# Kernel tuning notes

Hardware: AMD Instinct MI355X
Metric: run time of the kernel (lower is better)

## Reference

```python
import jax, jax.numpy as jnp
import numpy as np
from jax import lax

B, S, W = 64, 64, 12          # batch, sentences, words-per-sentence (max_seq)
V, SYM, HID = 32000, 128, 256  # vocab, symbol_size, hidden_size
E, R = 64, 32                  # entity_size, role_size
EPS = 1e-5


def _mlp(x, W1, b1, W2, b2):
    # equation 'b...e,er->b...r' is a matmul on the last axis; tanh hidden, linear out
    return jnp.tanh(x @ W1 + b1) @ W2 + b2


def _ln(x, g, b):
    mu = jnp.mean(x, axis=-1, keepdims=True)
    var = jnp.mean(jnp.square(x - mu), axis=-1, keepdims=True)
    return (x - mu) * lax.rsqrt(var + EPS) * g + b


def setup_inputs() -> dict:
    key = jax.random.key(0)
    ks = jax.random.split(key, 24)
    s_in = 1.0 / np.sqrt(SYM)
    s_h = 1.0 / np.sqrt(HID)
    inp = {
        "story": jax.random.randint(ks[0], (B, S, W), 0, V),
        "query": jax.random.randint(ks[1], (B, W), 0, V),
        "word_embed": jax.random.uniform(ks[2], (V, SYM), jnp.float32, -0.1, 0.1),
        "pos_embed": jnp.ones((W, SYM), jnp.float32) / W,
        # UpdateModule MLPs: 2 entity heads (out=E), 3 role heads (out=R), stacked
        "ue_W1": jax.random.normal(ks[3], (2, SYM, HID)) * s_in,
        "ue_b1": jnp.zeros((2, HID), jnp.float32),
        "ue_W2": jax.random.normal(ks[4], (2, HID, E)) * s_h,
        "ue_b2": jnp.zeros((2, E), jnp.float32),
        "ur_W1": jax.random.normal(ks[5], (3, SYM, HID)) * s_in,
        "ur_b1": jnp.zeros((3, HID), jnp.float32),
        "ur_W2": jax.random.normal(ks[6], (3, HID, R)) * s_h,
        "ur_b2": jnp.zeros((3, R), jnp.float32),
        # InferenceModule MLPs
        "ie_W1": jax.random.normal(ks[7], (2, SYM, HID)) * s_in,
        "ie_b1": jnp.zeros((2, HID), jnp.float32),
        "ie_W2": jax.random.normal(ks[8], (2, HID, E)) * s_h,
        "ie_b2": jnp.zeros((2, E), jnp.float32),
        "ir_W1": jax.random.normal(ks[9], (3, SYM, HID)) * s_in,
        "ir_b1": jnp.zeros((3, HID), jnp.float32),
        "ir_W2": jax.random.normal(ks[10], (3, HID, R)) * s_h,
        "ir_b2": jnp.zeros((3, R), jnp.float32),
        "ln_g": jnp.ones((3, E), jnp.float32),
        "ln_b": jnp.zeros((3, E), jnp.float32),
        "Z": jax.random.normal(ks[11], (E, V)) * (1.0 / np.sqrt(E)),
    }
    return inp


def reference(story, query, word_embed, pos_embed,
              ue_W1, ue_b1, ue_W2, ue_b2, ur_W1, ur_b1, ur_W2, ur_b2,
              ie_W1, ie_b1, ie_W2, ie_b2, ir_W1, ir_b1, ir_W2, ir_b2,
              ln_g, ln_b, Z):
    # ---- InputModule ----
    sent = jnp.einsum('bswe,we->bse', word_embed[story], pos_embed)   # [B,S,SYM]
    qsum = jnp.einsum('bwe,we->be', word_embed[query], pos_embed)     # [B,SYM]

    # ---- UpdateModule: precompute per-step entity/role vectors ----
    e1 = _mlp(sent, ue_W1[0], ue_b1[0], ue_W2[0], ue_b2[0])  # [B,S,E]
    e2 = _mlp(sent, ue_W1[1], ue_b1[1], ue_W2[1], ue_b2[1])
    r1 = _mlp(sent, ur_W1[0], ur_b1[0], ur_W2[0], ur_b2[0])  # [B,S,R]
    r2 = _mlp(sent, ur_W1[1], ur_b1[1], ur_W2[1], ur_b2[1])
    r3 = _mlp(sent, ur_W1[2], ur_b1[2], ur_W2[2], ur_b2[2])
    paW = jnp.einsum('bsr,bsf->bsrf', r1, e2)
    paB = jnp.einsum('bsr,bsf->bsrf', r3, e1)

    xs = tuple(jnp.moveaxis(t, 1, 0) for t in (e1, r1, paW, e2, r2, paB, r3))

    def step(TPR, x):
        e1i, r1i, paWi, e2i, r2i, paBi, r3i = x
        t1 = jnp.einsum('be,berf->brf', e1i, TPR)
        w_hat = jnp.einsum('br,brf->bf', r1i, t1)
        m_hat = jnp.einsum('br,brf->bf', r2i, t1)
        b_hat = jnp.einsum('be,br,berf->bf', e2i, r3i, TPR)
        write_op = paWi - r1i[:, :, None] * w_hat[:, None, :]
        move_op = r2i[:, :, None] * (w_hat - m_hat)[:, None, :]
        back_op = paBi - r3i[:, :, None] * b_hat[:, None, :]
        delta = (jnp.einsum('be,brf->berf', e1i, write_op + move_op)
                 + jnp.einsum('be,brf->berf', e2i, back_op))
        return TPR + delta, None

    TPR0 = jnp.zeros((sent.shape[0], E, R, E), sent.dtype)
    TPR, _ = lax.scan(step, TPR0, xs)

    # ---- InferenceModule ----
    qe1 = _mlp(qsum, ie_W1[0], ie_b1[0], ie_W2[0], ie_b2[0])
    qr1 = _mlp(qsum, ir_W1[0], ir_b1[0], ir_W2[0], ir_b2[0])
    qr2 = _mlp(qsum, ir_W1[1], ir_b1[1], ir_W2[1], ir_b2[1])
    qr3 = _mlp(qsum, ir_W1[2], ir_b1[2], ir_W2[2], ir_b2[2])
    i1 = _ln(jnp.einsum('be,br,berf->bf', qe1, qr1, TPR), ln_g[0], ln_b[0])
    i2 = _ln(jnp.einsum('be,br,berf->bf', i1, qr2, TPR), ln_g[1], ln_b[1])
    i3 = _ln(jnp.einsum('be,br,berf->bf', i2, qr3, TPR), ln_g[2], ln_b[2])
    return (i1 + i2 + i3) @ Z
```

## Files before the change

### kernel.cpp

```cpp
#include <hip/hip_runtime.h>
#include <math.h>

#define B_   64
#define S_   64
#define W_   12
#define V_   32000
#define SYM_ 128
#define HID_ 256
#define E_   64
#define R_   32

__global__ __launch_bounds__(128) void k_embed(
    const int* __restrict__ story, const int* __restrict__ query,
    const float* __restrict__ we, const float* __restrict__ pe,
    float* __restrict__ X) {
  int row = blockIdx.x;
  int e = threadIdx.x;
  const int* idx = (row < 4096) ? story + row * W_ : query + (row - 4096) * W_;
  float acc = 0.f;
#pragma unroll
  for (int w = 0; w < W_; ++w)
    acc = fmaf(we[(long)idx[w] * SYM_ + e], pe[w * SYM_ + e], acc);
  X[row * SYM_ + e] = acc;
}

__global__ __launch_bounds__(256) void k_mlp(
    const float* __restrict__ X,
    const float* __restrict__ ueW1, const float* __restrict__ ueb1,
    const float* __restrict__ ueW2, const float* __restrict__ ueb2,
    const float* __restrict__ urW1, const float* __restrict__ urb1,
    const float* __restrict__ urW2, const float* __restrict__ urb2,
    const float* __restrict__ ieW1, const float* __restrict__ ieb1,
    const float* __restrict__ ieW2, const float* __restrict__ ieb2,
    const float* __restrict__ irW1, const float* __restrict__ irb1,
    const float* __restrict__ irW2, const float* __restrict__ irb2,
    float* __restrict__ oE0, float* __restrict__ oE1,
    float* __restrict__ oR0, float* __restrict__ oR1, float* __restrict__ oR2) {
  __shared__ float SM[9472];
  float* W1L = SM + 1280;

  int h = blockIdx.x % 5;
  int tile = blockIdx.x / 5;
  int rowbase = tile * 32;
  bool isQ = (rowbase >= 4096);
  bool isE = (h < 2);
  const float* W1 = isE ? (isQ ? ieW1 : ueW1) + h * (SYM_ * HID_)
                        : (isQ ? irW1 : urW1) + (h - 2) * (SYM_ * HID_);
  const float* b1 = isE ? (isQ ? ieb1 : ueb1) + h * HID_
                        : (isQ ? irb1 : urb1) + (h - 2) * HID_;
  const float* W2 = isE ? (isQ ? ieW2 : ueW2) + h * (HID_ * E_)
                        : (isQ ? irW2 : urW2) + (h - 2) * (HID_ * R_);
  const float* b2 = isE ? (isQ ? ieb2 : ueb2) + h * E_
                        : (isQ ? irb2 : urb2) + (h - 2) * R_;
  float* out = (h == 0) ? oE0 : (h == 1) ? oE1 : (h == 2) ? oR0 : (h == 3) ? oR1 : oR2;

  int tid = threadIdx.x;
  int wv = tid >> 6;
  int l = tid & 63;

  float a[8][4];
#pragma unroll
  for (int i = 0; i < 8; ++i)
#pragma unroll
    for (int q = 0; q < 4; ++q) a[i][q] = 0.f;

  for (int kc = 0; kc < 4; ++kc) {
    __syncthreads();
    {
      int row = tid >> 3, k4 = (tid & 7) * 4;
      float4 v = *(const float4*)(X + (long)(rowbase + row) * SYM_ + kc * 32 + k4);
      SM[(k4 + 0) * 40 + row] = v.x;
      SM[(k4 + 1) * 40 + row] = v.y;
      SM[(k4 + 2) * 40 + row] = v.z;
      SM[(k4 + 3) * 40 + row] = v.w;
    }
    {
      const float* src = W1 + kc * 32 * HID_;
#pragma unroll
      for (int t = 0; t < 8; ++t)
        *(float4*)&W1L[(tid + 256 * t) * 4] = *(const float4*)(src + (tid + 256 * t) * 4);
    }
    __syncthreads();
#pragma unroll 4
    for (int k = 0; k < 32; ++k) {
      float4 wvv = *(const float4*)&W1L[k * 256 + 4 * l];
      float4 x0 = *(const float4*)&SM[k * 40 + 8 * wv];
      float4 x1 = *(const float4*)&SM[k * 40 + 8 * wv + 4];
      float xs[8] = {x0.x, x0.y, x0.z, x0.w, x1.x, x1.y, x1.z, x1.w};
#pragma unroll
      for (int i = 0; i < 8; ++i) {
        a[i][0] = fmaf(xs[i], wvv.x, a[i][0]);
        a[i][1] = fmaf(xs[i], wvv.y, a[i][1]);
        a[i][2] = fmaf(xs[i], wvv.z, a[i][2]);
        a[i][3] = fmaf(xs[i], wvv.w, a[i][3]);
      }
    }
  }
  __syncthreads();
  {
    float4 b1v = *(const float4*)(b1 + 4 * l);
#pragma unroll
    for (int i = 0; i < 8; ++i) {
      float4 hv = make_float4(tanhf(a[i][0] + b1v.x), tanhf(a[i][1] + b1v.y),
                              tanhf(a[i][2] + b1v.z), tanhf(a[i][3] + b1v.w));
      *(float4*)&SM[(8 * wv + i) * 260 + 4 * l] = hv;
    }
  }
  __syncthreads();
  if (isE) {
    float acc[8];
#pragma unroll
    for (int i = 0; i < 8; ++i) acc[i] = 0.f;
#pragma unroll 2
    for (int c4 = 0; c4 < 64; ++c4) {
      float w0 = W2[(long)(4 * c4 + 0) * E_ + l];
      float w1 = W2[(long)(4 * c4 + 1) * E_ + l];
      float w2 = W2[(long)(4 * c4 + 2) * E_ + l];
      float w3 = W2[(long)(4 * c4 + 3) * E_ + l];
#pragma unroll
      for (int i = 0; i < 8; ++i) {
        float4 hh = *(const float4*)&SM[(8 * wv + i) * 260 + 4 * c4];
        acc[i] = fmaf(hh.x, w0, fmaf(hh.y, w1, fmaf(hh.z, w2, fmaf(hh.w, w3, acc[i]))));
      }
    }
    float bb = b2[l];
#pragma unroll
    for (int i = 0; i < 8; ++i)
      out[(long)(rowbase + 8 * wv + i) * E_ + l] = acc[i] + bb;
  } else {
    int lc = l & 31;
    float acc[8];
#pragma unroll
    for (int i = 0; i < 8; ++i) acc[i] = 0.f;
#pragma unroll 2
    for (int c4 = 0; c4 < 64; ++c4) {
      float w0 = W2[(long)(4 * c4 + 0) * R_ + lc];
      float w1 = W2[(long)(4 * c4 + 1) * R_ + lc];
      float w2 = W2[(long)(4 * c4 + 2) * R_ + lc];
      float w3 = W2[(long)(4 * c4 + 3) * R_ + lc];
#pragma unroll
      for (int i = 0; i < 8; ++i) {
        float4 hh = *(const float4*)&SM[(8 * wv + i) * 260 + 4 * c4];
        acc[i] = fmaf(hh.x, w0, fmaf(hh.y, w1, fmaf(hh.z, w2, fmaf(hh.w, w3, acc[i]))));
      }
    }
    if (l < 32) {
      float bb = b2[lc];
#pragma unroll
      for (int i = 0; i < 8; ++i)
        out[(long)(rowbase + 8 * wv + i) * R_ + lc] = acc[i] + bb;
    }
  }
}

__global__ __launch_bounds__(256) void k_gram(
    const float* __restrict__ e1, const float* __restrict__ e2,
    const float* __restrict__ r1, const float* __restrict__ r2,
    const float* __restrict__ r3, float* __restrict__ Wt) {
  int b = blockIdx.x / 9, m = blockIdx.x % 9;
  const float* sE = ((m < 6) ? e1 : e2) + (long)b * S_ * E_;
  const float* jE = ((m == 2 || m == 5 || m == 8) ? e2 : e1) + (long)b * S_ * E_;
  int sk = m / 3, jk = m % 3;
  const float* sR = ((sk == 0) ? r1 : (sk == 1) ? r2 : r3) + (long)b * S_ * R_;
  const float* jR = ((jk == 0) ? r1 : (jk == 1) ? r2 : r3) + (long)b * S_ * R_;

  __shared__ float Es[64][68], Ej[64][68], Rs[64][36], Rj[64][36];
  int tid = threadIdx.x;
  for (int i = tid; i < 1024; i += 256) {
    int row = i >> 4, c = i & 15;
    *(float4*)&Es[row][4 * c] = *(const float4*)(sE + row * 64 + 4 * c);
    *(float4*)&Ej[row][4 * c] = *(const float4*)(jE + row * 64 + 4 * c);
  }
  for (int i = tid; i < 512; i += 256) {
    int row = i >> 3, c = i & 7;
    *(float4*)&Rs[row][4 * c] = *(const float4*)(sR + row * 32 + 4 * c);
    *(float4*)&Rj[row][4 * c] = *(const float4*)(jR + row * 32 + 4 * c);
  }
  __syncthreads();

  int s0 = (tid & 15) * 4, j0 = (tid >> 4) * 4;
  float ed[4][4] = {}, rd[4][4] = {};
#pragma unroll 4
  for (int k = 0; k < 16; ++k) {
    float4 es[4], ej[4];
#pragma unroll
    for (int i = 0; i < 4; ++i) {
      es[i] = *(const float4*)&Es[s0 + i][4 * k];
      ej[i] = *(const float4*)&Ej[j0 + i][4 * k];
    }
#pragma unroll
    for (int i = 0; i < 4; ++i)
#pragma unroll
      for (int j = 0; j < 4; ++j)
        ed[i][j] = fmaf(es[i].x, ej[j].x, fmaf(es[i].y, ej[j].y,
                   fmaf(es[i].z, ej[j].z, fmaf(es[i].w, ej[j].w, ed[i][j]))));
  }
#pragma unroll 4
  for (int k = 0; k < 8; ++k) {
    float4 rs[4], rj[4];
#pragma unroll
    for (int i = 0; i < 4; ++i) {
      rs[i] = *(const float4*)&Rs[s0 + i][4 * k];
      rj[i] = *(const float4*)&Rj[j0 + i][4 * k];
    }
#pragma unroll
    for (int i = 0; i < 4; ++i)
#pragma unroll
      for (int j = 0; j < 4; ++j)
        rd[i][j] = fmaf(rs[i].x, rj[j].x, fmaf(rs[i].y, rj[j].y,
                   fmaf(rs[i].z, rj[j].z, fmaf(rs[i].w, rj[j].w, rd[i][j]))));
  }
  float* wout = Wt + (long)(b * 9 + m) * 4096;
#pragma unroll
  for (int jj = 0; jj < 4; ++jj) {
    float4 o4 = make_float4(ed[0][jj] * rd[0][jj], ed[1][jj] * rd[1][jj],
                            ed[2][jj] * rd[2][jj], ed[3][jj] * rd[3][jj]);
    *(float4*)(wout + (j0 + jj) * 64 + s0) = o4;
  }
}

__global__ __launch_bounds__(256) void k_scan(
    const float* __restrict__ e1g, const float* __restrict__ e2g,
    const float* __restrict__ Wt, float4* __restrict__ acd) {
  __shared__ float WtL[9 * 512];
  int b = blockIdx.x & 63;
  int g = blockIdx.x >> 6;
  int tid = threadIdx.x;
  int wv = tid >> 6;
  int lane = tid & 63;
  int f0 = g * 8 + wv * 2;
  int f1 = f0 + 1;
  const float* Wb = Wt + (long)b * 9 * 4096;
  long eoff = ((long)b * 64 + lane) * 64;
  float e1x = e1g[eoff + f0], e1y = e1g[eoff + f1];
  float e2x = e2g[eoff + f0], e2y = e2g[eoff + f1];

  float pW0 = 0.f, pM0 = 0.f, pB0 = 0.f;
  float pW1 = 0.f, pM1 = 0.f, pB1 = 0.f;
  float ca0 = e2x, cc0 = 0.f, cd0 = e1x;
  float ca1 = e2y, cc1 = 0.f, cd1 = e1y;
  float ka0 = 0.f, kc0 = 0.f, kd0 = 0.f;
  float ka1 = 0.f, kc1 = 0.f, kd1 = 0.f;

  for (int jc = 0; jc < 8; ++jc) {
    __syncthreads();
    for (int i = tid; i < 1152; i += 256) {
      int m = i >> 7;
      int off = (i & 127) * 4;
      *(float4*)&WtL[m * 512 + off] = *(const float4*)(Wb + m * 4096 + jc * 512 + off);
    }
    __syncthreads();
#pragma unroll
    for (int jj = 0; jj < 8; ++jj) {
      int j = jc * 8 + jj;
      float wa = WtL[0 * 512 + jj * 64 + lane];
      float wc = WtL[1 * 512 + jj * 64 + lane];
      float wd = WtL[2 * 512 + jj * 64 + lane];
      float ma = WtL[3 * 512 + jj * 64 + lane];
      float mc = WtL[4 * 512 + jj * 64 + lane];
      float md = WtL[5 * 512 + jj * 64 + lane];
      float ba = WtL[6 * 512 + jj * 64 + lane];
      float bc = WtL[7 * 512 + jj * 64 + lane];
      float bd = WtL[8 * 512 + jj * 64 + lane];
      float aj0 = __int_as_float(__builtin_amdgcn_readlane(__float_as_int(ca0), j));
      float cj0 = __int_as_float(__builtin_amdgcn_readlane(__float_as_int(cc0), j));
      float dj0 = __int_as_float(__builtin_amdgcn_readlane(__float_as_int(cd0), j));
      float aj1 = __int_as_float(__builtin_amdgcn_readlane(__float_as_int(ca1), j));
      float cj1 = __int_as_float(__builtin_amdgcn_readlane(__float_as_int(cc1), j));
      float dj1 = __int_as_float(__builtin_amdgcn_readlane(__float_as_int(cd1), j));
      bool own = (lane == j);
      ka0 = own ? ca0 : ka0; kc0 = own ? cc0 : kc0; kd0 = own ? cd0 : kd0;
      ka1 = own ? ca1 : ka1; kc1 = own ? cc1 : kc1; kd1 = own ? cd1 : kd1;
      pW0 = fmaf(wa, aj0, pW0); pW0 = fmaf(wc, cj0, pW0); pW0 = fmaf(wd, dj0, pW0);
      pM0 = fmaf(ma, aj0, pM0); pM0 = fmaf(mc, cj0, pM0); pM0 = fmaf(md, dj0, pM0);
      pB0 = fmaf(ba, aj0, pB0); pB0 = fmaf(bc, cj0, pB0); pB0 = fmaf(bd, dj0, pB0);
      pW1 = fmaf(wa, aj1, pW1); pW1 = fmaf(wc, cj1, pW1); pW1 = fmaf(wd, dj1, pW1);
      pM1 = fmaf(ma, aj1, pM1); pM1 = fmaf(mc, cj1, pM1); pM1 = fmaf(md, dj1, pM1);
      pB1 = fmaf(ba, aj1, pB1); pB1 = fmaf(bc, cj1, pB1); pB1 = fmaf(bd, dj1, pB1);
      ca0 = e2x - pW0; cc0 = pW0 - pM0; cd0 = e1x - pB0;
      ca1 = e2y - pW1; cc1 = pW1 - pM1; cd1 = e1y - pB1;
    }
  }
  acd[eoff + f0] = make_float4(ka0, kc0, kd0, 0.f);
  acd[eoff + f1] = make_float4(ka1, kc1, kd1, 0.f);
}

__global__ __launch_bounds__(1024) void k_infer(
    const float4* __restrict__ acd,
    const float* __restrict__ e1, const float* __restrict__ e2,
    const float* __restrict__ r1, const float* __restrict__ r2,
    const float* __restrict__ r3,
    const float* __restrict__ qe1, const float* __restrict__ qr1,
    const float* __restrict__ qr2, const float* __restrict__ qr3,
    const float* __restrict__ lng, const float* __restrict__ lnb,
    float* __restrict__ isum) {
  int b = blockIdx.x, tid = threadIdx.x;
  __shared__ float hista[64 * 65], histc[64 * 65], histd[64 * 65];
  __shared__ float vlds[9 * 64];
  __shared__ float ivec[64];
  __shared__ float u1s[64], u2s[64];
  __shared__ float dsc[64];

  {
    const float4* ab = acd + (long)b * 4096;
    for (int idx = tid; idx < 4096; idx += 1024) {
      float4 hv = ab[idx];
      int j = idx >> 6, f = idx & 63;
      hista[j * 65 + f] = hv.x;
      histc[j * 65 + f] = hv.y;
      histd[j * 65 + f] = hv.z;
    }
  }
  if (tid < 576) {
    int pk = tid >> 6, j = tid & 63;
    int p = pk / 3, k = pk % 3;
    const float* rv = ((k == 0) ? r1 : (k == 1) ? r2 : r3) + ((long)b * 64 + j) * 32;
    const float* q = ((p == 0) ? qr1 : (p == 1) ? qr2 : qr3) + b * 32;
    float acc = 0.f;
#pragma unroll
    for (int t = 0; t < 8; ++t) {
      float4 rv4 = *(const float4*)(rv + 4 * t);
      float4 q4 = *(const float4*)(q + 4 * t);
      acc = fmaf(rv4.x, q4.x, fmaf(rv4.y, q4.y,
            fmaf(rv4.z, q4.z, fmaf(rv4.w, q4.w, acc))));
    }
    vlds[pk * 64 + j] = acc;
  }
  if (tid < 64) ivec[tid] = qe1[b * 64 + tid];
  __syncthreads();

  int f = tid >> 4, jsl = tid & 15;
  int dotd = tid >> 3, dt = tid & 7;
  int which = dotd >> 6, dj = dotd & 63;
  const float* erow = (which ? e2 : e1) + ((long)b * 64 + dj) * 64 + dt * 8;
  float isacc = 0.f;
  for (int p = 0; p < 3; ++p) {
    {
      float acc = 0.f;
#pragma unroll
      for (int t = 0; t < 8; ++t)
        acc = fmaf(erow[t], ivec[dt * 8 + t], acc);
      acc += __shfl_xor(acc, 1, 64);
      acc += __shfl_xor(acc, 2, 64);
      acc += __shfl_xor(acc, 4, 64);
      if (dt == 0) { if (which) u2s[dj] = acc; else u1s[dj] = acc; }
    }
    __syncthreads();
    float part = 0.f;
#pragma unroll
    for (int i = 0; i < 4; ++i) {
      int j = jsl * 4 + i;
      float ca = u1s[j] * vlds[(p * 3 + 0) * 64 + j];
      float cc = u1s[j] * vlds[(p * 3 + 1) * 64 + j];
      float cd = u2s[j] * vlds[(p * 3 + 2) * 64 + j];
      part = fmaf(ca, hista[j * 65 + f],
             fmaf(cc, histc[j * 65 + f],
             fmaf(cd, histd[j * 65 + f], part)));
    }
    part += __shfl_xor(part, 1, 64);
    part += __shfl_xor(part, 2, 64);
    part += __shfl_xor(part, 4, 64);
    part += __shfl_xor(part, 8, 64);
    if (jsl == 0) dsc[f] = part;
    __syncthreads();
    if (tid < 64) {
      float v = dsc[tid];
      float mu = v;
#pragma unroll
      for (int mm = 1; mm <= 32; mm <<= 1) mu += __shfl_xor(mu, mm, 64);
      mu *= (1.f / 64.f);
      float d = v - mu;
      float vr = d * d;
#pragma unroll
      for (int mm = 1; mm <= 32; mm <<= 1) vr += __shfl_xor(vr, mm, 64);
      vr *= (1.f / 64.f);
      float iv = d * (1.f / sqrtf(vr + 1e-5f)) * lng[p * 64 + tid] + lnb[p * 64 + tid];
      ivec[tid] = iv;
      isacc += iv;
    }
    __syncthreads();
  }
  if (tid < 64) isum[b * 64 + tid] = isacc;
}

__global__ __launch_bounds__(256) void k_final(
    const float* __restrict__ isum, const float* __restrict__ Zm,
    float* __restrict__ out) {
  __shared__ float isT[64 * 68];
  int tid = threadIdx.x;
  for (int i = tid; i < 4096; i += 256) {
    int bb = i >> 6, e = i & 63;
    isT[e * 68 + bb] = isum[i];
  }
  __syncthreads();
  int tr = tid >> 4, tc = tid & 15;
  int v0 = blockIdx.x * 64 + tc * 4;
  float acc[4][4] = {};
#pragma unroll 2
  for (int e = 0; e < 64; ++e) {
    float4 a4 = *(const float4*)&isT[e * 68 + 4 * tr];
    float4 z4 = *(const float4*)(Zm + (long)e * V_ + v0);
    float as[4] = {a4.x, a4.y, a4.z, a4.w};
    float zs[4] = {z4.x, z4.y, z4.z, z4.w};
#pragma unroll
    for (int i = 0; i < 4; ++i)
#pragma unroll
      for (int j = 0; j < 4; ++j) acc[i][j] = fmaf(as[i], zs[j], acc[i][j]);
  }
#pragma unroll
  for (int i = 0; i < 4; ++i) {
    float4 o4 = make_float4(acc[i][0], acc[i][1], acc[i][2], acc[i][3]);
    *(float4*)(out + (long)(4 * tr + i) * V_ + v0) = o4;
  }
}

extern "C" void kernel_launch(void* const* d_in, const int* in_sizes, int n_in,
                              void* d_out, int out_size, void* d_ws, size_t ws_size,
                              hipStream_t stream) {
  const int* story = (const int*)d_in[0];
  const int* query = (const int*)d_in[1];
  const float* we = (const float*)d_in[2];
  const float* pe = (const float*)d_in[3];
  const float* ueW1 = (const float*)d_in[4];
  const float* ueb1 = (const float*)d_in[5];
  const float* ueW2 = (const float*)d_in[6];
  const float* ueb2 = (const float*)d_in[7];
  const float* urW1 = (const float*)d_in[8];
  const float* urb1 = (const float*)d_in[9];
  const float* urW2 = (const float*)d_in[10];
  const float* urb2 = (const float*)d_in[11];
  const float* ieW1 = (const float*)d_in[12];
  const float* ieb1 = (const float*)d_in[13];
  const float* ieW2 = (const float*)d_in[14];
  const float* ieb2 = (const float*)d_in[15];
  const float* irW1 = (const float*)d_in[16];
  const float* irb1 = (const float*)d_in[17];
  const float* irW2 = (const float*)d_in[18];
  const float* irb2 = (const float*)d_in[19];
  const float* lng = (const float*)d_in[20];
  const float* lnb = (const float*)d_in[21];
  const float* Zm = (const float*)d_in[22];

  float* ws = (float*)d_ws;
  float* X = ws;
  float* e1 = X + 532480;
  float* e2 = e1 + 266240;
  float* r1 = e2 + 266240;
  float* r2 = r1 + 133120;
  float* r3 = r2 + 133120;
  float* isum = r3 + 133120;
  float* Wt = isum + 4096;
  float4* acd = (float4*)(Wt + 2359296);
  float* qe1 = e1 + 4096 * 64;
  float* qr1 = r1 + 4096 * 32;
  float* qr2 = r2 + 4096 * 32;
  float* qr3 = r3 + 4096 * 32;
  float* outF = (float*)d_out;

  k_embed<<<4160, 128, 0, stream>>>(story, query, we, pe, X);
  k_mlp<<<130 * 5, 256, 0, stream>>>(X, ueW1, ueb1, ueW2, ueb2,
                                     urW1, urb1, urW2, urb2,
                                     ieW1, ieb1, ieW2, ieb2,
                                     irW1, irb1, irW2, irb2,
                                     e1, e2, r1, r2, r3);
  k_gram<<<64 * 9, 256, 0, stream>>>(e1, e2, r1, r2, r3, Wt);
  k_scan<<<512, 256, 0, stream>>>(e1, e2, Wt, acd);
  k_infer<<<B_, 1024, 0, stream>>>(acd, e1, e2, r1, r2, r3, qe1, qr1, qr2, qr3,
                                   lng, lnb, isum);
  k_final<<<V_ / 64, 256, 0, stream>>>(isum, Zm, outF);
}
```

Before: 221.9 us.

## Stage full X tile in LDS once and stream W1 directly from global

The first MLP layer now loads the whole 32x128 input tile into shared memory once, in row-major layout with padding. W1 is no longer staged through LDS in four chunks. Each thread instead reads its float4 W1 columns directly from global memory (likely L2-cached), which removes the per-chunk barriers and the W1 LDS traffic. The cost is more global load latency on W1, with less shared memory used per block.

Measured after the change: 220.6 us. Within noise of the previous version (-0.6%).

```diff
diff --git a/kernel.cpp b/kernel.cpp
--- a/kernel.cpp
+++ b/kernel.cpp
@@ -36,8 +36,7 @@
     const float* __restrict__ irW2, const float* __restrict__ irb2,
     float* __restrict__ oE0, float* __restrict__ oE1,
     float* __restrict__ oR0, float* __restrict__ oR1, float* __restrict__ oR2) {
-  __shared__ float SM[9472];
-  float* W1L = SM + 1280;
+  __shared__ float SM[8320];
 
   int h = blockIdx.x % 5;
   int tile = blockIdx.x / 5;
@@ -58,42 +57,49 @@
   int wv = tid >> 6;
   int l = tid & 63;
 
+#pragma unroll
+  for (int c = 0; c < 4; ++c) {
+    int i = tid + 256 * c;
+    int row = i >> 5, k4 = (i & 31) * 4;
+    *(float4*)&SM[row * 136 + k4] = *(const float4*)(X + (long)(rowbase + row) * SYM_ + k4);
+  }
+  __syncthreads();
+
   float a[8][4];
 #pragma unroll
   for (int i = 0; i < 8; ++i)
 #pragma unroll
     for (int q = 0; q < 4; ++q) a[i][q] = 0.f;
 
-  for (int kc = 0; kc < 4; ++kc) {
-    __syncthreads();
-    {
-      int row = tid >> 3, k4 = (tid & 7) * 4;
-      float4 v = *(const float4*)(X + (long)(rowbase + row) * SYM_ + kc * 32 + k4);
-      SM[(k4 + 0) * 40 + row] = v.x;
-      SM[(k4 + 1) * 40 + row] = v.y;
-      SM[(k4 + 2) * 40 + row] = v.z;
-      SM[(k4 + 3) * 40 + row] = v.w;
-    }
-    {
-      const float* src = W1 + kc * 32 * HID_;
-#pragma unroll
-      for (int t = 0; t < 8; ++t)
-        *(float4*)&W1L[(tid + 256 * t) * 4] = *(const float4*)(src + (tid + 256 * t) * 4);
-    }
-    __syncthreads();
-#pragma unroll 4
-    for (int k = 0; k < 32; ++k) {
-      float4 wvv = *(const float4*)&W1L[k * 256 + 4 * l];
-      float4 x0 = *(const float4*)&SM[k * 40 + 8 * wv];
-      float4 x1 = *(const float4*)&SM[k * 40 + 8 * wv + 4];
-      float xs[8] = {x0.x, x0.y, x0.z, x0.w, x1.x, x1.y, x1.z, x1.w};
-#pragma unroll
-      for (int i = 0; i < 8; ++i) {
-        a[i][0] = fmaf(xs[i], wvv.x, a[i][0]);
-        a[i][1] = fmaf(xs[i], wvv.y, a[i][1]);
-        a[i][2] = fmaf(xs[i], wvv.z, a[i][2]);
-        a[i][3] = fmaf(xs[i], wvv.w, a[i][3]);
-      }
+  const float* W1p = W1 + 4 * l;
+#pragma unroll 2
+  for (int kg = 0; kg < 32; ++kg) {
+    float4 w0 = *(const float4*)(W1p + (long)(4 * kg + 0) * HID_);
+    float4 w1 = *(const float4*)(W1p + (long)(4 * kg + 1) * HID_);
+    float4 w2 = *(const float4*)(W1p + (long)(4 * kg + 2) * HID_);
+    float4 w3 = *(const float4*)(W1p + (long)(4 * kg + 3) * HID_);
+    float4 xr[8];
+#pragma unroll
+    for (int i = 0; i < 8; ++i)
+      xr[i] = *(const float4*)&SM[(8 * wv + i) * 136 + 4 * kg];
+#pragma unroll
+    for (int i = 0; i < 8; ++i) {
+      a[i][0] = fmaf(xr[i].x, w0.x, a[i][0]);
+      a[i][1] = fmaf(xr[i].x, w0.y, a[i][1]);
+      a[i][2] = fmaf(xr[i].x, w0.z, a[i][2]);
+      a[i][3] = fmaf(xr[i].x, w0.w, a[i][3]);
+      a[i][0] = fmaf(xr[i].y, w1.x, a[i][0]);
+      a[i][1] = fmaf(xr[i].y, w1.y, a[i][1]);
+      a[i][2] = fmaf(xr[i].y, w1.z, a[i][2]);
+      a[i][3] = fmaf(xr[i].y, w1.w, a[i][3]);
+      a[i][0] = fmaf(xr[i].z, w2.x, a[i][0]);
+      a[i][1] = fmaf(xr[i].z, w2.y, a[i][1]);
+      a[i][2] = fmaf(xr[i].z, w2.z, a[i][2]);
+      a[i][3] = fmaf(xr[i].z, w2.w, a[i][3]);
+      a[i][0] = fmaf(xr[i].w, w3.x, a[i][0]);
+      a[i][1] = fmaf(xr[i].w, w3.y, a[i][1]);
+      a[i][2] = fmaf(xr[i].w, w3.z, a[i][2]);
+      a[i][3] = fmaf(xr[i].w, w3.w, a[i][3]);
     }
   }
   __syncthreads();
```
